# Performance work log

Hardware: AMD Instinct MI355X
Metric: run time of the kernel (lower is better)

The kernel has to match this reference:

```python
import jax, jax.numpy as jnp
import numpy as np

B, N, D2, S = 64, 4096, 128, 512  # b, n, 2*d, size_s


def setup_inputs() -> dict:
    key = jax.random.key(0)
    k1, k2, k3, k4 = jax.random.split(key, 4)
    s_past = jax.random.randint(k1, (B, N), 0, S)
    yq = jax.random.normal(k2, (B, 1, D2), dtype=jnp.float32)
    y_past = jax.random.normal(k3, (B, N, D2), dtype=jnp.float32)
    w_mat = jax.random.normal(k4, (D2, D2), dtype=jnp.float32)
    return {"s_past": s_past, "yq": yq, "y_past": y_past, "w_mat": w_mat, "size_s": S}


def reference(s_past, yq, y_past, w_mat, size_s):
    # attn_logits[b,n] = yq[b,0,:] @ w_mat @ y_past[b,n,:]
    attn_logits = jnp.einsum('bqd,de,bne->bn', yq, w_mat, y_past)
    attn = jax.nn.softmax(attn_logits, axis=-1)  # (b, n)
    b, n = s_past.shape
    # post_est[b, s] = sum_n attn[b, n] * [s_past[b, n] == s]
    # fused scatter-add instead of materializing one-hot (b, n, S)
    flat_ids = (s_past + size_s * jnp.arange(b, dtype=s_past.dtype)[:, None]).reshape(-1)
    post_est = jax.ops.segment_sum(attn.reshape(-1), flat_ids,
                                   num_segments=b * size_s).reshape(b, size_s)
    return post_est
```

## Files before the change

### kernel.cpp

```cpp
#include <hip/hip_runtime.h>
#include <math.h>

#define BB 64
#define NN 4096
#define DD 128
#define SS 512
#define CHUNKS 16
#define RPC 256
#define SUBT 4

__global__ __launch_bounds__(256, 4) void fused_kernel(
    const float* __restrict__ y_past, const float* __restrict__ yq,
    const float* __restrict__ w, const int* __restrict__ s_past,
    float* __restrict__ bins_g, float* __restrict__ pmax) {
    const int b = blockIdx.x, chunk = blockIdx.y;
    const int t = threadIdx.x;
    const int j = t & 3;
    const int r = t >> 2;

    __shared__ float syq[DD];
    __shared__ float qsh[DD];
    __shared__ float bins[SS];
    __shared__ float wred[8];

    const float4* gp =
        (const float4*)y_past + ((size_t)b * NN + (size_t)chunk * RPC) * 32;

    float4 y0[4];
#pragma unroll
    for (int k = 0; k < 4; ++k) y0[k] = gp[(size_t)r * 32 + j * 8 + k];

    int sreg[SUBT];
    if (j == 0) {
#pragma unroll
        for (int s = 0; s < SUBT; ++s)
            sreg[s] = s_past[(size_t)b * NN + chunk * RPC + s * 64 + r];
    }

    if (t < DD) syq[t] = yq[b * DD + t];
    bins[t] = 0.f;
    bins[t + 256] = 0.f;
    __syncthreads();

    if (t < DD) {
        float acc = 0.f;
#pragma unroll
        for (int d = 0; d < DD; ++d) acc = fmaf(syq[d], w[d * DD + t], acc);
        qsh[t] = acc;
    }
    __syncthreads();

    float4 qreg[8];
#pragma unroll
    for (int k = 0; k < 8; ++k) qreg[k] = ((const float4*)qsh)[j * 8 + k];

    float pv[SUBT];

    {
        float4 acc = {0.f, 0.f, 0.f, 0.f};
#pragma unroll
        for (int k = 0; k < 4; ++k) {
            acc.x = fmaf(qreg[k].x, y0[k].x, acc.x);
            acc.y = fmaf(qreg[k].y, y0[k].y, acc.y);
            acc.z = fmaf(qreg[k].z, y0[k].z, acc.z);
            acc.w = fmaf(qreg[k].w, y0[k].w, acc.w);
        }
#pragma unroll
        for (int k = 4; k < 8; ++k) {
            float4 yv = gp[(size_t)r * 32 + j * 8 + k];
            acc.x = fmaf(qreg[k].x, yv.x, acc.x);
            acc.y = fmaf(qreg[k].y, yv.y, acc.y);
            acc.z = fmaf(qreg[k].z, yv.z, acc.z);
            acc.w = fmaf(qreg[k].w, yv.w, acc.w);
        }
        float p = (acc.x + acc.y) + (acc.z + acc.w);
        p += __shfl_xor(p, 1, 64);
        p += __shfl_xor(p, 2, 64);
        pv[0] = p;
    }

#pragma unroll
    for (int s = 1; s < SUBT; ++s) {
        float4 acc = {0.f, 0.f, 0.f, 0.f};
#pragma unroll
        for (int k = 0; k < 8; ++k) {
            float4 yv = gp[(size_t)(s * 64 + r) * 32 + j * 8 + k];
            acc.x = fmaf(qreg[k].x, yv.x, acc.x);
            acc.y = fmaf(qreg[k].y, yv.y, acc.y);
            acc.z = fmaf(qreg[k].z, yv.z, acc.z);
            acc.w = fmaf(qreg[k].w, yv.w, acc.w);
        }
        float p = (acc.x + acc.y) + (acc.z + acc.w);
        p += __shfl_xor(p, 1, 64);
        p += __shfl_xor(p, 2, 64);
        pv[s] = p;
    }

    float m = fmaxf(fmaxf(pv[0], pv[1]), fmaxf(pv[2], pv[3]));
#pragma unroll
    for (int off = 32; off > 0; off >>= 1) m = fmaxf(m, __shfl_xor(m, off, 64));
    int wave = t >> 6, lane = t & 63;
    if (lane == 0) wred[wave] = m;
    __syncthreads();
    m = fmaxf(fmaxf(wred[0], wred[1]), fmaxf(wred[2], wred[3]));

    if (j == 0) {
#pragma unroll
        for (int s = 0; s < SUBT; ++s)
            atomicAdd(&bins[sreg[s]], __expf(pv[s] - m));
    }
    __syncthreads();

    float* bg = bins_g + ((size_t)b * CHUNKS + chunk) * SS;
    bg[t] = bins[t];
    bg[t + 256] = bins[t + 256];
    if (t == 0) pmax[b * CHUNKS + chunk] = m;
}

__global__ __launch_bounds__(512) void combine_kernel(
    const float* __restrict__ bins_g, const float* __restrict__ pmax,
    float* __restrict__ out) {
    int b = blockIdx.x;
    int t = threadIdx.x;
    __shared__ float scale[CHUNKS];
    __shared__ float red[8];
    __shared__ float sInv;

    if (t < CHUNKS) scale[t] = pmax[b * CHUNKS + t];
    __syncthreads();
    if (t == 0) {
        float M = scale[0];
#pragma unroll
        for (int c = 1; c < CHUNKS; ++c) M = fmaxf(M, scale[c]);
#pragma unroll
        for (int c = 0; c < CHUNKS; ++c) scale[c] = __expf(scale[c] - M);
    }
    __syncthreads();

    float acc = 0.f;
#pragma unroll
    for (int c = 0; c < CHUNKS; ++c)
        acc = fmaf(bins_g[((size_t)b * CHUNKS + c) * SS + t], scale[c], acc);

    float s = acc;
#pragma unroll
    for (int off = 32; off > 0; off >>= 1) s += __shfl_xor(s, off, 64);
    if ((t & 63) == 0) red[t >> 6] = s;
    __syncthreads();
    if (t == 0) {
        float S = 0.f;
#pragma unroll
        for (int i = 0; i < 8; ++i) S += red[i];
        sInv = 1.f / S;
    }
    __syncthreads();

    out[b * SS + t] = acc * sInv;
}

extern "C" void kernel_launch(void* const* d_in, const int* in_sizes, int n_in,
                              void* d_out, int out_size, void* d_ws, size_t ws_size,
                              hipStream_t stream) {
    const int*   s_past = (const int*)d_in[0];
    const float* yq     = (const float*)d_in[1];
    const float* y_past = (const float*)d_in[2];
    const float* w_mat  = (const float*)d_in[3];

    float* ws     = (float*)d_ws;
    float* bins_g = ws;
    float* pmax   = bins_g + BB * CHUNKS * SS;
    float* out    = (float*)d_out;

    fused_kernel<<<dim3(BB, CHUNKS), 256, 0, stream>>>(y_past, yq, w_mat,
                                                       s_past, bins_g, pmax);
    combine_kernel<<<BB, SS, 0, stream>>>(bins_g, pmax, out);
}
```

Baseline: 206.6 us.

## Prefetch all y_past rows into registers before the query projection

```diff
diff --git a/kernel.cpp b/kernel.cpp
--- a/kernel.cpp
+++ b/kernel.cpp
@@ -9,7 +9,7 @@
 #define RPC 256
 #define SUBT 4
 
-__global__ __launch_bounds__(256, 4) void fused_kernel(
+__global__ __launch_bounds__(256, 2) void fused_kernel(
     const float* __restrict__ y_past, const float* __restrict__ yq,
     const float* __restrict__ w, const int* __restrict__ s_past,
     float* __restrict__ bins_g, float* __restrict__ pmax) {
@@ -18,7 +18,6 @@
     const int j = t & 3;
     const int r = t >> 2;
 
-    __shared__ float syq[DD];
     __shared__ float qsh[DD];
     __shared__ float bins[SS];
     __shared__ float wred[8];
@@ -26,9 +25,12 @@
     const float4* gp =
         (const float4*)y_past + ((size_t)b * NN + (size_t)chunk * RPC) * 32;
 
-    float4 y0[4];
+    float4 yv[SUBT][8];
 #pragma unroll
-    for (int k = 0; k < 4; ++k) y0[k] = gp[(size_t)r * 32 + j * 8 + k];
+    for (int s = 0; s < SUBT; ++s)
+#pragma unroll
+        for (int k = 0; k < 8; ++k)
+            yv[s][k] = gp[(size_t)(s * 64 + r) * 32 + j * 8 + k];
 
     int sreg[SUBT];
     if (j == 0) {
@@ -37,58 +39,36 @@
             sreg[s] = s_past[(size_t)b * NN + chunk * RPC + s * 64 + r];
     }
 
-    if (t < DD) syq[t] = yq[b * DD + t];
     bins[t] = 0.f;
     bins[t + 256] = 0.f;
-    __syncthreads();
+
+    __builtin_amdgcn_sched_barrier(0);
 
     if (t < DD) {
+        const float* yqb = yq + b * DD;
         float acc = 0.f;
 #pragma unroll
-        for (int d = 0; d < DD; ++d) acc = fmaf(syq[d], w[d * DD + t], acc);
+        for (int d = 0; d < DD; ++d) acc = fmaf(yqb[d], w[d * DD + t], acc);
         qsh[t] = acc;
     }
-    __syncthreads();
+
+    asm volatile("s_waitcnt lgkmcnt(0)" ::: "memory");
+    __builtin_amdgcn_s_barrier();
 
     float4 qreg[8];
 #pragma unroll
     for (int k = 0; k < 8; ++k) qreg[k] = ((const float4*)qsh)[j * 8 + k];
 
     float pv[SUBT];
-
-    {
-        float4 acc = {0.f, 0.f, 0.f, 0.f};
 #pragma unroll
-        for (int k = 0; k < 4; ++k) {
-            acc.x = fmaf(qreg[k].x, y0[k].x, acc.x);
-            acc.y = fmaf(qreg[k].y, y0[k].y, acc.y);
-            acc.z = fmaf(qreg[k].z, y0[k].z, acc.z);
-            acc.w = fmaf(qreg[k].w, y0[k].w, acc.w);
-        }
-#pragma unroll
-        for (int k = 4; k < 8; ++k) {
-            float4 yv = gp[(size_t)r * 32 + j * 8 + k];
-            acc.x = fmaf(qreg[k].x, yv.x, acc.x);
-            acc.y = fmaf(qreg[k].y, yv.y, acc.y);
-            acc.z = fmaf(qreg[k].z, yv.z, acc.z);
-            acc.w = fmaf(qreg[k].w, yv.w, acc.w);
-        }
-        float p = (acc.x + acc.y) + (acc.z + acc.w);
-        p += __shfl_xor(p, 1, 64);
-        p += __shfl_xor(p, 2, 64);
-        pv[0] = p;
-    }
-
-#pragma unroll
-    for (int s = 1; s < SUBT; ++s) {
+    for (int s = 0; s < SUBT; ++s) {
         float4 acc = {0.f, 0.f, 0.f, 0.f};
 #pragma unroll
         for (int k = 0; k < 8; ++k) {
-            float4 yv = gp[(size_t)(s * 64 + r) * 32 + j * 8 + k];
-            acc.x = fmaf(qreg[k].x, yv.x, acc.x);
-            acc.y = fmaf(qreg[k].y, yv.y, acc.y);
-            acc.z = fmaf(qreg[k].z, yv.z, acc.z);
-            acc.w = fmaf(qreg[k].w, yv.w, acc.w);
+            acc.x = fmaf(qreg[k].x, yv[s][k].x, acc.x);
+            acc.y = fmaf(qreg[k].y, yv[s][k].y, acc.y);
+            acc.z = fmaf(qreg[k].z, yv[s][k].z, acc.z);
+            acc.w = fmaf(qreg[k].w, yv[s][k].w, acc.w);
         }
         float p = (acc.x + acc.y) + (acc.z + acc.w);
         p += __shfl_xor(p, 1, 64);
@@ -99,7 +79,7 @@
     float m = fmaxf(fmaxf(pv[0], pv[1]), fmaxf(pv[2], pv[3]));
 #pragma unroll
     for (int off = 32; off > 0; off >>= 1) m = fmaxf(m, __shfl_xor(m, off, 64));
-    int wave = t >> 6, lane = t & 63;
+    const int wave = t >> 6, lane = t & 63;
     if (lane == 0) wred[wave] = m;
     __syncthreads();
     m = fmaxf(fmaxf(wred[0], wred[1]), fmaxf(wred[2], wred[3]));
```

New measurement: 267.8 us. +29.6%, slower.
